# Kernel tuning notes

Measured on AMD Instinct MI355X. Metric: run time of the kernel, lower is better.

Reference implementation:

```python
import jax, jax.numpy as jnp
import numpy as np

NUM_NODES = 200000  # num_user + num_item
DIM_E = 64
NUM_EDGES = 600000
EPS = 1e-12
NEG_SLOPE = 0.01  # F.leaky_relu default


def setup_inputs() -> dict:
    key = jax.random.key(0)
    k1, k2, k3 = jax.random.split(key, 3)
    # xavier_normal on [N, D]: std = sqrt(2/(fan_in+fan_out))
    std = float(np.sqrt(2.0 / (NUM_NODES + DIM_E)))
    id_embedding = jax.random.normal(k1, (NUM_NODES, DIM_E), dtype=jnp.float32) * std
    edge_index = jax.random.randint(k2, (2, NUM_EDGES), 0, NUM_NODES, dtype=jnp.int64)
    weight_vector = jax.random.uniform(k3, (2 * NUM_EDGES, 1), dtype=jnp.float32)
    return {"id_embedding": id_embedding, "edge_index": edge_index,
            "weight_vector": weight_vector}


def _l2_normalize(x):
    # F.normalize(x, p=2, dim=1, eps=1e-12)
    n = jnp.sqrt(jnp.sum(x * x, axis=1, keepdims=True))
    return x / jnp.maximum(n, EPS)


def _leaky_relu(x):
    return jnp.where(x >= 0, x, NEG_SLOPE * x)


def reference(id_embedding, edge_index, weight_vector):
    N = id_embedding.shape[0]
    # symmetrize: cat(edge_index, edge_index[[1,0]])
    ei = jnp.concatenate([edge_index, edge_index[::-1]], axis=1)
    src, dst = ei[0], ei[1]  # messages flow src -> dst (PyG source_to_target)
    cnt = jax.ops.segment_sum(jnp.ones((src.shape[0],), jnp.float32), dst,
                              num_segments=N)[:, None]
    denom = jnp.maximum(cnt, 1.0)  # isolated nodes: sum is 0, mean defined as 0

    def conv(x):
        msg = x[src] * weight_vector            # gather + per-edge scale [2E, D]
        agg = jax.ops.segment_sum(msg, dst, num_segments=N)  # scatter-sum [N, D]
        return agg / denom                      # scatter-mean

    x = _l2_normalize(id_embedding)
    x1 = _leaky_relu(conv(x))
    x2 = _leaky_relu(conv(x1))
    return x + x1 + x2
```

## Files before the change

kernel.cpp:

```cpp
#include <hip/hip_runtime.h>
#include <hip/hip_fp16.h>

#define DIM 64
#define NEG_SLOPE 0.01f
#define BKT 256
#define TILEP 4096
#define RECS (TILEP * 2)
#define STILE 2048

typedef unsigned u32;
typedef unsigned short u16;
typedef unsigned char u8;


__global__ void k_norm_hist(const float* __restrict__ emb,
                            __half* __restrict__ x0h,
                            const int* __restrict__ p,
                            u32* __restrict__ mat,
                            int N, int E, int rb, int B, int nblkE) {
    int t = threadIdx.x;
    if ((int)blockIdx.x < rb) {
        int lane = t & 63;
        int row  = blockIdx.x * 32 + (t >> 6) * 4 + (lane >> 4);
        int l16  = lane & 15;
        if (row >= N) return;
        float4 v = *(const float4*)(emb + (size_t)row * DIM + l16 * 4);
        float s = v.x * v.x + v.y * v.y + v.z * v.z + v.w * v.w;
        #pragma unroll
        for (int m = 1; m < 16; m <<= 1) s += __shfl_xor(s, m, 64);
        float inv = 1.0f / fmaxf(sqrtf(s), 1e-12f);
        union { uint2 u; __half2 h[2]; } pk;
        pk.h[0] = __floats2half2_rn(v.x * inv, v.y * inv);
        pk.h[1] = __floats2half2_rn(v.z * inv, v.w * inv);
        *(uint2*)(x0h + (size_t)row * DIM + l16 * 4) = pk.u;
    } else {
        __shared__ u32 hist[800];
        int blk = blockIdx.x - rb;
        for (int i = t; i < B; i += 512) hist[i] = 0;
        __syncthreads();
        int base = blk * TILEP;
        #pragma unroll
        for (int k = 0; k < TILEP / 512; k++) {
            int pe = base + k * 512 + t;
            if (pe < E) {
                int a = p[pe];
                int b = p[pe + E];
                atomicAdd(&hist[(u32)b >> 8], 1u);
                atomicAdd(&hist[(u32)a >> 8], 1u);
            }
        }
        __syncthreads();
        for (int i = t; i < B; i += 512) mat[(size_t)i * nblkE + blk] = hist[i];
    }
}

__global__ void k_scan1(const u32* __restrict__ in, u32* __restrict__ out,
                        u32* __restrict__ bsum, int M) {
    __shared__ u32 sdata[256];
    int t = threadIdx.x;
    int base = blockIdx.x * STILE + t * 8;
    u32 v[8]; u32 tsum = 0;
    #pragma unroll
    for (int k = 0; k < 8; k++) {
        int i = base + k;
        v[k] = (i < M) ? in[i] : 0u;
        tsum += v[k];
    }
    sdata[t] = tsum;
    __syncthreads();
    for (int off = 1; off < 256; off <<= 1) {
        u32 x = (t >= off) ? sdata[t - off] : 0u;
        __syncthreads();
        sdata[t] += x;
        __syncthreads();
    }
    u32 run = sdata[t] - tsum;
    if (t == 255) bsum[blockIdx.x] = sdata[255];
    #pragma unroll
    for (int k = 0; k < 8; k++) {
        int i = base + k;
        if (i < M) out[i] = run;
        run += v[k];
    }
}

__global__ void k_scanfix(u32* __restrict__ mscan,
                          const u32* __restrict__ bsum, int nb, int M) {
    __shared__ u32 sdata[256];
    __shared__ u32 sexcl[256];
    int t = threadIdx.x;
    u32 v = (t < nb) ? bsum[t] : 0u;
    sdata[t] = v;
    __syncthreads();
    for (int off = 1; off < 256; off <<= 1) {
        u32 x = (t >= off) ? sdata[t - off] : 0u;
        __syncthreads();
        sdata[t] += x;
        __syncthreads();
    }
    sexcl[t] = sdata[t] - v;
    __syncthreads();
    int i = blockIdx.x * 256 + t;
    if (i < M) mscan[i] += sexcl[i >> 11];
}

__global__ __launch_bounds__(512, 1)
void k_place(const int* __restrict__ p, const float* __restrict__ w,
             const u32* __restrict__ mscan,
             u32* __restrict__ pay, u8* __restrict__ loc8,
             int E, int nblkE, int B) {
    __shared__ u32 sPay[RECS];
    __shared__ u32 sMeta[RECS];
    __shared__ u16 sPerm[RECS];
    __shared__ u32 hist[1024];
    __shared__ u32 sstart[1024];
    __shared__ u32 delta[1024];
    __shared__ u32 sdata[512];

    int blk = blockIdx.x;
    int t = threadIdx.x;
    int base = blk * TILEP;
    int rem = E - base;
    int vlim = rem * 2; if (vlim > RECS) vlim = RECS;

    hist[t] = 0; hist[t + 512] = 0;
    __syncthreads();

    #pragma unroll
    for (int k = 0; k < TILEP / 512; k++) {
        int pe = base + k * 512 + t;
        if (pe < E) {
            int a = p[pe];
            int b = p[pe + E];
            float wf = w[pe];
            float wb = w[pe + E];
            u32 wf14 = (u32)(wf * 16384.0f + 0.5f); if (wf14 > 16383u) wf14 = 16383u;
            u32 wb14 = (u32)(wb * 16384.0f + 0.5f); if (wb14 > 16383u) wb14 = 16383u;
            int li = (k * 512 + t) * 2;
            sPay[li]      = ((u32)a << 14) | wf14;
            sMeta[li]     = (u32)b;
            sPay[li + 1]  = ((u32)b << 14) | wb14;
            sMeta[li + 1] = (u32)a;
            atomicAdd(&hist[(u32)b >> 8], 1u);
            atomicAdd(&hist[(u32)a >> 8], 1u);
        }
    }
    __syncthreads();

    u32 a0 = hist[2 * t], a1 = hist[2 * t + 1];
    u32 tsum = a0 + a1;
    sdata[t] = tsum;
    __syncthreads();
    for (int off = 1; off < 512; off <<= 1) {
        u32 x = (t >= off) ? sdata[t - off] : 0u;
        __syncthreads();
        sdata[t] += x;
        __syncthreads();
    }
    u32 texcl = sdata[t] - tsum;
    sstart[2 * t]     = texcl;
    sstart[2 * t + 1] = texcl + a0;
    __syncthreads();

    hist[t] = 0; hist[t + 512] = 0;
    for (int i = t; i < B; i += 512)
        delta[i] = mscan[(size_t)i * nblkE + blk] - sstart[i];
    __syncthreads();

    #pragma unroll
    for (int k = 0; k < RECS / 512; k++) {
        int li = k * 512 + t;
        if (li < vlim) {
            u32 bin = sMeta[li] >> 8;
            u32 r = atomicAdd(&hist[bin], 1u);
            sPerm[sstart[bin] + r] = (u16)li;
        }
    }
    __syncthreads();

    #pragma unroll
    for (int k = 0; k < RECS / 512; k++) {
        int j = k * 512 + t;
        if (j < vlim) {
            int li = sPerm[j];
            u32 pv = sPay[li];
            u32 mt = sMeta[li];
            u32 gs = (u32)j + delta[mt >> 8];
            pay[gs]  = pv;
            loc8[gs] = (u8)(mt & 255u);
        }
    }
}

__global__ void k_bucket(const u32* __restrict__ pay,
                         const u8* __restrict__ loc8,
                         const u32* __restrict__ mscan,
                         u32* __restrict__ row_ptr,
                         u32* __restrict__ colw,
                         int N, int E, int B, int nblkE) {
    __shared__ u32 hist[BKT];
    __shared__ u32 excl[BKT];
    __shared__ u32 sdata[256];
    int b = blockIdx.x;
    int t = threadIdx.x;
    int node0 = b * BKT;
    int nnodes = N - node0; if (nnodes > BKT) nnodes = BKT;
    size_t flat0 = (size_t)b * nblkE;
    u32 seg_s = mscan[flat0];
    u32 seg_e = (b + 1 < B) ? mscan[flat0 + nblkE] : (u32)(2 * E);
    hist[t] = 0;
    __syncthreads();
    for (u32 j = seg_s + t; j < seg_e; j += 256)
        atomicAdd(&hist[loc8[j]], 1u);
    __syncthreads();
    u32 tsum = hist[t];
    sdata[t] = tsum;
    __syncthreads();
    for (int off = 1; off < 256; off <<= 1) {
        u32 x = (t >= off) ? sdata[t - off] : 0u;
        __syncthreads();
        sdata[t] += x;
        __syncthreads();
    }
    u32 texcl = sdata[t] - tsum;
    excl[t] = texcl;
    if (t < nnodes) row_ptr[node0 + t] = seg_s + texcl;
    if (b == 0 && t == 0) row_ptr[N] = (u32)(2 * E);
    __syncthreads();
    for (u32 j = seg_s + t; j < seg_e; j += 256) {
        u32 loc = loc8[j];
        u32 pos = atomicAdd(&excl[loc], 1u);
        colw[seg_s + pos] = pay[j];
    }
}


__device__ __forceinline__ void gather8(const __half* __restrict__ x,
                                        const u32* __restrict__ colw,
                                        u32 s, u32 e, int g, int sub,
                                        float acc[8]) {
    for (u32 base = s; base < e; base += 8) {
        int m = (int)(e - base); if (m > 8) m = 8;
        u32 u = 0;
        if (sub < m) u = colw[base + sub];
        int   cx = (int)(u >> 14);
        float cy = (float)(u & 16383u) * (1.0f / 16384.0f);
        for (int j = 0; j < m; j++) {
            int   sj = __shfl(cx, (g << 3) | j, 64);
            float wj = __shfl(cy, (g << 3) | j, 64);
            uint4 q = *(const uint4*)(x + (size_t)sj * DIM + sub * 8);
            const __half2* hp = (const __half2*)&q;
            #pragma unroll
            for (int k = 0; k < 4; k++) {
                float2 f = __half22float2(hp[k]);
                acc[2 * k]     += f.x * wj;
                acc[2 * k + 1] += f.y * wj;
            }
        }
    }
}

__global__ void k_conv1(const __half* __restrict__ x0h,
                        const u32* __restrict__ row_ptr,
                        const u32* __restrict__ colw,
                        __half* __restrict__ x1h, int N) {
    int wave = (blockIdx.x * 256 + threadIdx.x) >> 6;
    int g    = (threadIdx.x >> 3) & 7;
    int sub  = threadIdx.x & 7;
    int row  = wave * 8 + g;
    if (row >= N) return;
    u32 s = row_ptr[row], e = row_ptr[row + 1];
    float acc[8] = {0, 0, 0, 0, 0, 0, 0, 0};
    gather8(x0h, colw, s, e, g, sub, acc);
    float rdeno = 1.0f / fmaxf((float)(e - s), 1.0f);
    __half2 hv[4];
    #pragma unroll
    for (int k = 0; k < 4; k++) {
        float v0 = acc[2 * k] * rdeno;
        float v1 = acc[2 * k + 1] * rdeno;
        v0 = (v0 >= 0.0f) ? v0 : NEG_SLOPE * v0;
        v1 = (v1 >= 0.0f) ? v1 : NEG_SLOPE * v1;
        hv[k] = __floats2half2_rn(v0, v1);
    }
    *(uint4*)(x1h + (size_t)row * DIM + sub * 8) = *(const uint4*)hv;
}

__global__ void k_conv2(const __half* __restrict__ x0h,
                        const __half* __restrict__ x1h,
                        const u32* __restrict__ row_ptr,
                        const u32* __restrict__ colw,
                        float* __restrict__ out, int N) {
    int wave = (blockIdx.x * 256 + threadIdx.x) >> 6;
    int g    = (threadIdx.x >> 3) & 7;
    int sub  = threadIdx.x & 7;
    int row  = wave * 8 + g;
    if (row >= N) return;
    u32 s = row_ptr[row], e = row_ptr[row + 1];
    float acc[8] = {0, 0, 0, 0, 0, 0, 0, 0};
    gather8(x1h, colw, s, e, g, sub, acc);
    float rdeno = 1.0f / fmaxf((float)(e - s), 1.0f);
    uint4 q0 = *(const uint4*)(x0h + (size_t)row * DIM + sub * 8);
    uint4 q1 = *(const uint4*)(x1h + (size_t)row * DIM + sub * 8);
    const __half2* h0 = (const __half2*)&q0;
    const __half2* h1 = (const __half2*)&q1;
    float r[8];
    #pragma unroll
    for (int k = 0; k < 4; k++) {
        float2 a = __half22float2(h0[k]);
        float2 b = __half22float2(h1[k]);
        float x2a = acc[2 * k] * rdeno;
        float x2b = acc[2 * k + 1] * rdeno;
        x2a = (x2a >= 0.0f) ? x2a : NEG_SLOPE * x2a;
        x2b = (x2b >= 0.0f) ? x2b : NEG_SLOPE * x2b;
        r[2 * k]     = a.x + b.x + x2a;
        r[2 * k + 1] = a.y + b.y + x2b;
    }
    float* op = out + (size_t)row * DIM + sub * 8;
    *(float4*)(op)     = make_float4(r[0], r[1], r[2], r[3]);
    *(float4*)(op + 4) = make_float4(r[4], r[5], r[6], r[7]);
}

static inline size_t align16(size_t x) { return (x + 15) & ~(size_t)15; }

extern "C" void kernel_launch(void* const* d_in, const int* in_sizes, int n_in,
                              void* d_out, int out_size, void* d_ws, size_t ws_size,
                              hipStream_t stream) {
    const int N = in_sizes[0] / DIM;
    const int E = in_sizes[1] / 2;

    const float* emb = (const float*)d_in[0];
    const int*   ei  = (const int*)d_in[1];
    const float* w   = (const float*)d_in[2];
    float*       out = (float*)d_out;

    const int B     = (N + BKT - 1) / BKT;
    const int nblkE = (E + TILEP - 1) / TILEP;
    const int M     = B * nblkE;
    const int nb1   = (M + STILE - 1) / STILE;
    const int rb    = (N + 31) / 32;
    const int cvb   = (N + 31) / 32;

    char* ws = (char*)d_ws;
    size_t off = 0;
    __half* x0h    = (__half*)(ws + off); off += align16((size_t)N * DIM * 2);
    __half* x1h    = (__half*)(ws + off); off += align16((size_t)N * DIM * 2);
    u32*    pay    = (u32*)(ws + off);    off += align16((size_t)2 * E * 4);
    u8*     loc8   = (u8*)(ws + off);     off += align16((size_t)2 * E);
    u32*    colw   = (u32*)(ws + off);    off += align16((size_t)2 * E * 4);
    u32*    mat    = (u32*)(ws + off);    off += align16((size_t)M * 4);
    u32*    mscan  = (u32*)(ws + off);    off += align16((size_t)M * 4);
    u32*    row_ptr= (u32*)(ws + off);    off += align16((size_t)(N + 1) * 4);
    u32*    bsum   = (u32*)(ws + off);    off += align16(256 * 4);

    k_norm_hist<<<rb + nblkE, 512, 0, stream>>>(emb, x0h, ei, mat, N, E, rb, B, nblkE);
    k_scan1  <<<nb1, 256, 0, stream>>>(mat, mscan, bsum, M);
    k_scanfix<<<(M + 255) / 256, 256, 0, stream>>>(mscan, bsum, nb1, M);
    k_place  <<<nblkE, 512, 0, stream>>>(ei, w, mscan, pay, loc8, E, nblkE, B);
    k_bucket <<<B, 256, 0, stream>>>(pay, loc8, mscan, row_ptr, colw, N, E, B, nblkE);

    k_conv1<<<cvb, 256, 0, stream>>>(x0h, row_ptr, colw, x1h, N);
    k_conv2<<<cvb, 256, 0, stream>>>(x0h, x1h, row_ptr, colw, out, N);
}
```

Before: 210.7 us.

## Sort rows by degree for balanced conv waves and unroll gather loads

Adds a degree histogram in the bucket kernel, a scan, and a counting-sort kernel that produces a row order grouped by degree, so each wave's eight rows have similar neighbour counts in both conv kernels. The gather loop now issues all eight neighbour loads before the FMAs, and conv2 hoists its self-row loads ahead of the gather, to raise memory-level parallelism. This adds two small kernels, an order indirection, and scattered output writes. It also always loads eight neighbours even when fewer are valid, reading padded index 0 with weight 0.

```diff
diff --git a/kernel.cpp b/kernel.cpp
--- a/kernel.cpp
+++ b/kernel.cpp
@@ -85,10 +85,12 @@
 }
 
 __global__ void k_scanfix(u32* __restrict__ mscan,
-                          const u32* __restrict__ bsum, int nb, int M) {
+                          const u32* __restrict__ bsum,
+                          u32* __restrict__ dhist, int nb, int M) {
     __shared__ u32 sdata[256];
     __shared__ u32 sexcl[256];
     int t = threadIdx.x;
+    if (blockIdx.x == 0) dhist[t] = 0;
     u32 v = (t < nb) ? bsum[t] : 0u;
     sdata[t] = v;
     __syncthreads();
@@ -197,10 +199,12 @@
                          const u32* __restrict__ mscan,
                          u32* __restrict__ row_ptr,
                          u32* __restrict__ colw,
+                         u32* __restrict__ dhist,
                          int N, int E, int B, int nblkE) {
     __shared__ u32 hist[BKT];
     __shared__ u32 excl[BKT];
     __shared__ u32 sdata[256];
+    __shared__ u32 dh[256];
     int b = blockIdx.x;
     int t = threadIdx.x;
     int node0 = b * BKT;
@@ -209,11 +213,13 @@
     u32 seg_s = mscan[flat0];
     u32 seg_e = (b + 1 < B) ? mscan[flat0 + nblkE] : (u32)(2 * E);
     hist[t] = 0;
+    dh[t] = 0;
     __syncthreads();
     for (u32 j = seg_s + t; j < seg_e; j += 256)
         atomicAdd(&hist[loc8[j]], 1u);
     __syncthreads();
     u32 tsum = hist[t];
+    if (t < nnodes) atomicAdd(&dh[tsum > 255u ? 255u : tsum], 1u);
     sdata[t] = tsum;
     __syncthreads();
     for (int off = 1; off < 256; off <<= 1) {
@@ -227,6 +233,7 @@
     if (t < nnodes) row_ptr[node0 + t] = seg_s + texcl;
     if (b == 0 && t == 0) row_ptr[N] = (u32)(2 * E);
     __syncthreads();
+    if (dh[t]) atomicAdd(&dhist[t], dh[t]);
     for (u32 j = seg_s + t; j < seg_e; j += 256) {
         u32 loc = loc8[j];
         u32 pos = atomicAdd(&excl[loc], 1u);
@@ -234,41 +241,113 @@
     }
 }
 
+__global__ void k_dscan(const u32* __restrict__ dhist, u32* __restrict__ dcur) {
+    __shared__ u32 sdata[256];
+    int t = threadIdx.x;
+    u32 v = dhist[t];
+    sdata[t] = v;
+    __syncthreads();
+    for (int off = 1; off < 256; off <<= 1) {
+        u32 x = (t >= off) ? sdata[t - off] : 0u;
+        __syncthreads();
+        sdata[t] += x;
+        __syncthreads();
+    }
+    dcur[t] = sdata[t] - v;
+}
+
+__global__ void k_dorder(const u32* __restrict__ rp, u32* __restrict__ dcur,
+                         u32* __restrict__ order, int N) {
+    __shared__ u32 lh[256];
+    __shared__ u32 lbase[256];
+    __shared__ u32 lcur[256];
+    int t = threadIdx.x;
+    lh[t] = 0;
+    __syncthreads();
+    int base = blockIdx.x * 2048;
+    u32 degv[8];
+    #pragma unroll
+    for (int k = 0; k < 8; k++) {
+        int i = base + k * 256 + t;
+        u32 d = 0;
+        if (i < N) {
+            d = rp[i + 1] - rp[i];
+            if (d > 255u) d = 255u;
+            atomicAdd(&lh[d], 1u);
+        }
+        degv[k] = d;
+    }
+    __syncthreads();
+    u32 c = lh[t];
+    lbase[t] = c ? atomicAdd(&dcur[t], c) : 0u;
+    lcur[t] = 0;
+    __syncthreads();
+    #pragma unroll
+    for (int k = 0; k < 8; k++) {
+        int i = base + k * 256 + t;
+        if (i < N) {
+            u32 d = degv[k];
+            u32 r = atomicAdd(&lcur[d], 1u);
+            order[lbase[d] + r] = (u32)i;
+        }
+    }
+}
+
+
+__device__ __forceinline__ void fma8(const uint4& q, float wj, float acc[8]) {
+    const __half2* hp = (const __half2*)&q;
+    #pragma unroll
+    for (int k = 0; k < 4; k++) {
+        float2 f = __half22float2(hp[k]);
+        acc[2 * k]     += f.x * wj;
+        acc[2 * k + 1] += f.y * wj;
+    }
+}
 
 __device__ __forceinline__ void gather8(const __half* __restrict__ x,
                                         const u32* __restrict__ colw,
                                         u32 s, u32 e, int g, int sub,
                                         float acc[8]) {
+    int lb = g << 3;
     for (u32 base = s; base < e; base += 8) {
         int m = (int)(e - base); if (m > 8) m = 8;
-        u32 u = 0;
-        if (sub < m) u = colw[base + sub];
+        u32 u = (sub < m) ? colw[base + sub] : 0u;
         int   cx = (int)(u >> 14);
         float cy = (float)(u & 16383u) * (1.0f / 16384.0f);
-        for (int j = 0; j < m; j++) {
-            int   sj = __shfl(cx, (g << 3) | j, 64);
-            float wj = __shfl(cy, (g << 3) | j, 64);
-            uint4 q = *(const uint4*)(x + (size_t)sj * DIM + sub * 8);
-            const __half2* hp = (const __half2*)&q;
-            #pragma unroll
-            for (int k = 0; k < 4; k++) {
-                float2 f = __half22float2(hp[k]);
-                acc[2 * k]     += f.x * wj;
-                acc[2 * k + 1] += f.y * wj;
-            }
-        }
+        int s0 = __shfl(cx, lb + 0, 64), s1 = __shfl(cx, lb + 1, 64);
+        int s2 = __shfl(cx, lb + 2, 64), s3 = __shfl(cx, lb + 3, 64);
+        int s4 = __shfl(cx, lb + 4, 64), s5 = __shfl(cx, lb + 5, 64);
+        int s6 = __shfl(cx, lb + 6, 64), s7 = __shfl(cx, lb + 7, 64);
+        uint4 q0 = *(const uint4*)(x + (size_t)s0 * DIM + sub * 8);
+        uint4 q1 = *(const uint4*)(x + (size_t)s1 * DIM + sub * 8);
+        uint4 q2 = *(const uint4*)(x + (size_t)s2 * DIM + sub * 8);
+        uint4 q3 = *(const uint4*)(x + (size_t)s3 * DIM + sub * 8);
+        uint4 q4 = *(const uint4*)(x + (size_t)s4 * DIM + sub * 8);
+        uint4 q5 = *(const uint4*)(x + (size_t)s5 * DIM + sub * 8);
+        uint4 q6 = *(const uint4*)(x + (size_t)s6 * DIM + sub * 8);
+        uint4 q7 = *(const uint4*)(x + (size_t)s7 * DIM + sub * 8);
+        float w0 = __shfl(cy, lb + 0, 64), w1 = __shfl(cy, lb + 1, 64);
+        float w2 = __shfl(cy, lb + 2, 64), w3 = __shfl(cy, lb + 3, 64);
+        float w4 = __shfl(cy, lb + 4, 64), w5 = __shfl(cy, lb + 5, 64);
+        float w6 = __shfl(cy, lb + 6, 64), w7 = __shfl(cy, lb + 7, 64);
+        fma8(q0, w0, acc); fma8(q1, w1, acc);
+        fma8(q2, w2, acc); fma8(q3, w3, acc);
+        fma8(q4, w4, acc); fma8(q5, w5, acc);
+        fma8(q6, w6, acc); fma8(q7, w7, acc);
     }
 }
 
 __global__ void k_conv1(const __half* __restrict__ x0h,
                         const u32* __restrict__ row_ptr,
                         const u32* __restrict__ colw,
+                        const u32* __restrict__ order,
                         __half* __restrict__ x1h, int N) {
     int wave = (blockIdx.x * 256 + threadIdx.x) >> 6;
     int g    = (threadIdx.x >> 3) & 7;
     int sub  = threadIdx.x & 7;
-    int row  = wave * 8 + g;
-    if (row >= N) return;
+    int idx  = wave * 8 + g;
+    if (idx >= N) return;
+    int row = (int)order[idx];
     u32 s = row_ptr[row], e = row_ptr[row + 1];
     float acc[8] = {0, 0, 0, 0, 0, 0, 0, 0};
     gather8(x0h, colw, s, e, g, sub, acc);
@@ -289,18 +368,20 @@
                         const __half* __restrict__ x1h,
                         const u32* __restrict__ row_ptr,
                         const u32* __restrict__ colw,
+                        const u32* __restrict__ order,
                         float* __restrict__ out, int N) {
     int wave = (blockIdx.x * 256 + threadIdx.x) >> 6;
     int g    = (threadIdx.x >> 3) & 7;
     int sub  = threadIdx.x & 7;
-    int row  = wave * 8 + g;
-    if (row >= N) return;
+    int idx  = wave * 8 + g;
+    if (idx >= N) return;
+    int row = (int)order[idx];
     u32 s = row_ptr[row], e = row_ptr[row + 1];
+    uint4 q0 = *(const uint4*)(x0h + (size_t)row * DIM + sub * 8);
+    uint4 q1 = *(const uint4*)(x1h + (size_t)row * DIM + sub * 8);
     float acc[8] = {0, 0, 0, 0, 0, 0, 0, 0};
     gather8(x1h, colw, s, e, g, sub, acc);
     float rdeno = 1.0f / fmaxf((float)(e - s), 1.0f);
-    uint4 q0 = *(const uint4*)(x0h + (size_t)row * DIM + sub * 8);
-    uint4 q1 = *(const uint4*)(x1h + (size_t)row * DIM + sub * 8);
     const __half2* h0 = (const __half2*)&q0;
     const __half2* h1 = (const __half2*)&q1;
     float r[8];
@@ -339,6 +420,7 @@
     const int nb1   = (M + STILE - 1) / STILE;
     const int rb    = (N + 31) / 32;
     const int cvb   = (N + 31) / 32;
+    const int ob    = (N + 2047) / 2048;
 
     char* ws = (char*)d_ws;
     size_t off = 0;
@@ -351,13 +433,18 @@
     u32*    mscan  = (u32*)(ws + off);    off += align16((size_t)M * 4);
     u32*    row_ptr= (u32*)(ws + off);    off += align16((size_t)(N + 1) * 4);
     u32*    bsum   = (u32*)(ws + off);    off += align16(256 * 4);
+    u32*    dhist  = (u32*)(ws + off);    off += align16(256 * 4);
+    u32*    dcur   = (u32*)(ws + off);    off += align16(256 * 4);
+    u32*    order  = (u32*)(ws + off);    off += align16((size_t)N * 4);
 
     k_norm_hist<<<rb + nblkE, 512, 0, stream>>>(emb, x0h, ei, mat, N, E, rb, B, nblkE);
     k_scan1  <<<nb1, 256, 0, stream>>>(mat, mscan, bsum, M);
-    k_scanfix<<<(M + 255) / 256, 256, 0, stream>>>(mscan, bsum, nb1, M);
+    k_scanfix<<<(M + 255) / 256, 256, 0, stream>>>(mscan, bsum, dhist, nb1, M);
     k_place  <<<nblkE, 512, 0, stream>>>(ei, w, mscan, pay, loc8, E, nblkE, B);
-    k_bucket <<<B, 256, 0, stream>>>(pay, loc8, mscan, row_ptr, colw, N, E, B, nblkE);
-
-    k_conv1<<<cvb, 256, 0, stream>>>(x0h, row_ptr, colw, x1h, N);
-    k_conv2<<<cvb, 256, 0, stream>>>(x0h, x1h, row_ptr, colw, out, N);
-}
+    k_bucket <<<B, 256, 0, stream>>>(pay, loc8, mscan, row_ptr, colw, dhist, N, E, B, nblkE);
+    k_dscan  <<<1, 256, 0, stream>>>(dhist, dcur);
+    k_dorder <<<ob, 256, 0, stream>>>(row_ptr, dcur, order, N);
+
+    k_conv1<<<cvb, 256, 0, stream>>>(x0h, row_ptr, colw, order, x1h, N);
+    k_conv2<<<cvb, 256, 0, stream>>>(x0h, x1h, row_ptr, colw, order, out, N);
+}
```

New measurement: 226.8 us. 1.08x slower.

## Process two rows per lane group with batched unrolled neighbor gathers

Applied to the files above, without the earlier changes.

Each 8-lane group in both conv kernels now owns two destination rows instead of one. The neighbor loop is fully unrolled to issue eight independent 16-byte row loads (four per row) before any FMA, replacing the serial per-neighbor load-then-accumulate loop. This exposes more memory-level parallelism in the latency-bound gather and halves the launched grid. The cost is padded lanes: when a row has fewer than eight remaining edges, the extra lanes still load node 0 with zero weight, and register use per thread rises.

```diff
diff --git a/kernel.cpp b/kernel.cpp
--- a/kernel.cpp
+++ b/kernel.cpp
@@ -235,28 +235,66 @@
 }
 
 
-__device__ __forceinline__ void gather8(const __half* __restrict__ x,
+__device__ __forceinline__ void fma8(const uint4& q, float wj, float acc[8]) {
+    const __half2* hp = (const __half2*)&q;
+    #pragma unroll
+    for (int k = 0; k < 4; k++) {
+        float2 f = __half22float2(hp[k]);
+        acc[2 * k]     += f.x * wj;
+        acc[2 * k + 1] += f.y * wj;
+    }
+}
+
+__device__ __forceinline__ void gather2(const __half* __restrict__ x,
                                         const u32* __restrict__ colw,
-                                        u32 s, u32 e, int g, int sub,
-                                        float acc[8]) {
-    for (u32 base = s; base < e; base += 8) {
-        int m = (int)(e - base); if (m > 8) m = 8;
-        u32 u = 0;
-        if (sub < m) u = colw[base + sub];
-        int   cx = (int)(u >> 14);
-        float cy = (float)(u & 16383u) * (1.0f / 16384.0f);
-        for (int j = 0; j < m; j++) {
-            int   sj = __shfl(cx, (g << 3) | j, 64);
-            float wj = __shfl(cy, (g << 3) | j, 64);
-            uint4 q = *(const uint4*)(x + (size_t)sj * DIM + sub * 8);
-            const __half2* hp = (const __half2*)&q;
-            #pragma unroll
-            for (int k = 0; k < 4; k++) {
-                float2 f = __half22float2(hp[k]);
-                acc[2 * k]     += f.x * wj;
-                acc[2 * k + 1] += f.y * wj;
-            }
+                                        u32 s0, u32 e0, u32 s1, u32 e1,
+                                        int g, int sub,
+                                        float accA[8], float accB[8]) {
+    int lb = g << 3;
+    u32 bA = s0, bB = s1;
+    while (bA < e0 || bB < e1) {
+        u32 uA = (bA + (u32)sub < e0 && bA < e0) ? colw[bA + sub] : 0u;
+        u32 uB = (bB + (u32)sub < e1 && bB < e1) ? colw[bB + sub] : 0u;
+        int   cxA = (int)(uA >> 14);
+        float cyA = (float)(uA & 16383u) * (1.0f / 16384.0f);
+        int   cxB = (int)(uB >> 14);
+        float cyB = (float)(uB & 16383u) * (1.0f / 16384.0f);
+        #pragma unroll
+        for (int h = 0; h < 2; h++) {
+            int j0 = h * 4;
+            int a0 = __shfl(cxA, lb + j0 + 0, 64), a1 = __shfl(cxA, lb + j0 + 1, 64);
+            int a2 = __shfl(cxA, lb + j0 + 2, 64), a3 = __shfl(cxA, lb + j0 + 3, 64);
+            int b0 = __shfl(cxB, lb + j0 + 0, 64), b1 = __shfl(cxB, lb + j0 + 1, 64);
+            int b2 = __shfl(cxB, lb + j0 + 2, 64), b3 = __shfl(cxB, lb + j0 + 3, 64);
+            uint4 qa0 = *(const uint4*)(x + (size_t)a0 * DIM + sub * 8);
+            uint4 qa1 = *(const uint4*)(x + (size_t)a1 * DIM + sub * 8);
+            uint4 qa2 = *(const uint4*)(x + (size_t)a2 * DIM + sub * 8);
+            uint4 qa3 = *(const uint4*)(x + (size_t)a3 * DIM + sub * 8);
+            uint4 qb0 = *(const uint4*)(x + (size_t)b0 * DIM + sub * 8);
+            uint4 qb1 = *(const uint4*)(x + (size_t)b1 * DIM + sub * 8);
+            uint4 qb2 = *(const uint4*)(x + (size_t)b2 * DIM + sub * 8);
+            uint4 qb3 = *(const uint4*)(x + (size_t)b3 * DIM + sub * 8);
+            float wa0 = __shfl(cyA, lb + j0 + 0, 64), wa1 = __shfl(cyA, lb + j0 + 1, 64);
+            float wa2 = __shfl(cyA, lb + j0 + 2, 64), wa3 = __shfl(cyA, lb + j0 + 3, 64);
+            float wb0 = __shfl(cyB, lb + j0 + 0, 64), wb1 = __shfl(cyB, lb + j0 + 1, 64);
+            float wb2 = __shfl(cyB, lb + j0 + 2, 64), wb3 = __shfl(cyB, lb + j0 + 3, 64);
+            fma8(qa0, wa0, accA); fma8(qa1, wa1, accA);
+            fma8(qa2, wa2, accA); fma8(qa3, wa3, accA);
+            fma8(qb0, wb0, accB); fma8(qb1, wb1, accB);
+            fma8(qb2, wb2, accB); fma8(qb3, wb3, accB);
         }
+        bA += 8; bB += 8;
+    }
+}
+
+__device__ __forceinline__ void finish1(float acc[8], float rdeno, __half2 hv[4]) {
+    #pragma unroll
+    for (int k = 0; k < 4; k++) {
+        float v0 = acc[2 * k] * rdeno;
+        float v1 = acc[2 * k + 1] * rdeno;
+        v0 = (v0 >= 0.0f) ? v0 : NEG_SLOPE * v0;
+        v1 = (v1 >= 0.0f) ? v1 : NEG_SLOPE * v1;
+        hv[k] = __floats2half2_rn(v0, v1);
     }
 }
 
@@ -267,43 +305,28 @@
     int wave = (blockIdx.x * 256 + threadIdx.x) >> 6;
     int g    = (threadIdx.x >> 3) & 7;
     int sub  = threadIdx.x & 7;
-    int row  = wave * 8 + g;
-    if (row >= N) return;
-    u32 s = row_ptr[row], e = row_ptr[row + 1];
-    float acc[8] = {0, 0, 0, 0, 0, 0, 0, 0};
-    gather8(x0h, colw, s, e, g, sub, acc);
-    float rdeno = 1.0f / fmaxf((float)(e - s), 1.0f);
+    int r0   = wave * 16 + g * 2;
+    int r1   = r0 + 1;
+    if (r0 >= N) return;
+    u32 s0 = row_ptr[r0], e0 = row_ptr[r0 + 1];
+    u32 s1 = 0, e1 = 0;
+    if (r1 < N) { s1 = row_ptr[r1]; e1 = row_ptr[r1 + 1]; }
+    float accA[8] = {0,0,0,0,0,0,0,0};
+    float accB[8] = {0,0,0,0,0,0,0,0};
+    gather2(x0h, colw, s0, e0, s1, e1, g, sub, accA, accB);
     __half2 hv[4];
-    #pragma unroll
-    for (int k = 0; k < 4; k++) {
-        float v0 = acc[2 * k] * rdeno;
-        float v1 = acc[2 * k + 1] * rdeno;
-        v0 = (v0 >= 0.0f) ? v0 : NEG_SLOPE * v0;
-        v1 = (v1 >= 0.0f) ? v1 : NEG_SLOPE * v1;
-        hv[k] = __floats2half2_rn(v0, v1);
-    }
-    *(uint4*)(x1h + (size_t)row * DIM + sub * 8) = *(const uint4*)hv;
-}
-
-__global__ void k_conv2(const __half* __restrict__ x0h,
-                        const __half* __restrict__ x1h,
-                        const u32* __restrict__ row_ptr,
-                        const u32* __restrict__ colw,
-                        float* __restrict__ out, int N) {
-    int wave = (blockIdx.x * 256 + threadIdx.x) >> 6;
-    int g    = (threadIdx.x >> 3) & 7;
-    int sub  = threadIdx.x & 7;
-    int row  = wave * 8 + g;
-    if (row >= N) return;
-    u32 s = row_ptr[row], e = row_ptr[row + 1];
-    float acc[8] = {0, 0, 0, 0, 0, 0, 0, 0};
-    gather8(x1h, colw, s, e, g, sub, acc);
-    float rdeno = 1.0f / fmaxf((float)(e - s), 1.0f);
-    uint4 q0 = *(const uint4*)(x0h + (size_t)row * DIM + sub * 8);
-    uint4 q1 = *(const uint4*)(x1h + (size_t)row * DIM + sub * 8);
+    finish1(accA, 1.0f / fmaxf((float)(e0 - s0), 1.0f), hv);
+    *(uint4*)(x1h + (size_t)r0 * DIM + sub * 8) = *(const uint4*)hv;
+    if (r1 < N) {
+        finish1(accB, 1.0f / fmaxf((float)(e1 - s1), 1.0f), hv);
+        *(uint4*)(x1h + (size_t)r1 * DIM + sub * 8) = *(const uint4*)hv;
+    }
+}
+
+__device__ __forceinline__ void finish2(const uint4& q0, const uint4& q1,
+                                        float acc[8], float rdeno, float r[8]) {
     const __half2* h0 = (const __half2*)&q0;
     const __half2* h1 = (const __half2*)&q1;
-    float r[8];
     #pragma unroll
     for (int k = 0; k < 4; k++) {
         float2 a = __half22float2(h0[k]);
@@ -315,9 +338,43 @@
         r[2 * k]     = a.x + b.x + x2a;
         r[2 * k + 1] = a.y + b.y + x2b;
     }
-    float* op = out + (size_t)row * DIM + sub * 8;
+}
+
+__global__ void k_conv2(const __half* __restrict__ x0h,
+                        const __half* __restrict__ x1h,
+                        const u32* __restrict__ row_ptr,
+                        const u32* __restrict__ colw,
+                        float* __restrict__ out, int N) {
+    int wave = (blockIdx.x * 256 + threadIdx.x) >> 6;
+    int g    = (threadIdx.x >> 3) & 7;
+    int sub  = threadIdx.x & 7;
+    int r0   = wave * 16 + g * 2;
+    int r1   = r0 + 1;
+    if (r0 >= N) return;
+    u32 s0 = row_ptr[r0], e0 = row_ptr[r0 + 1];
+    u32 s1 = 0, e1 = 0;
+    if (r1 < N) { s1 = row_ptr[r1]; e1 = row_ptr[r1 + 1]; }
+    uint4 qa0 = *(const uint4*)(x0h + (size_t)r0 * DIM + sub * 8);
+    uint4 qa1 = *(const uint4*)(x1h + (size_t)r0 * DIM + sub * 8);
+    uint4 qb0, qb1;
+    if (r1 < N) {
+        qb0 = *(const uint4*)(x0h + (size_t)r1 * DIM + sub * 8);
+        qb1 = *(const uint4*)(x1h + (size_t)r1 * DIM + sub * 8);
+    }
+    float accA[8] = {0,0,0,0,0,0,0,0};
+    float accB[8] = {0,0,0,0,0,0,0,0};
+    gather2(x1h, colw, s0, e0, s1, e1, g, sub, accA, accB);
+    float r[8];
+    finish2(qa0, qa1, accA, 1.0f / fmaxf((float)(e0 - s0), 1.0f), r);
+    float* op = out + (size_t)r0 * DIM + sub * 8;
     *(float4*)(op)     = make_float4(r[0], r[1], r[2], r[3]);
     *(float4*)(op + 4) = make_float4(r[4], r[5], r[6], r[7]);
+    if (r1 < N) {
+        finish2(qb0, qb1, accB, 1.0f / fmaxf((float)(e1 - s1), 1.0f), r);
+        op = out + (size_t)r1 * DIM + sub * 8;
+        *(float4*)(op)     = make_float4(r[0], r[1], r[2], r[3]);
+        *(float4*)(op + 4) = make_float4(r[4], r[5], r[6], r[7]);
+    }
 }
 
 static inline size_t align16(size_t x) { return (x + 15) & ~(size_t)15; }
@@ -338,7 +395,7 @@
     const int M     = B * nblkE;
     const int nb1   = (M + STILE - 1) / STILE;
     const int rb    = (N + 31) / 32;
-    const int cvb   = (N + 31) / 32;
+    const int cvb   = (N + 63) / 64;
 
     char* ws = (char*)d_ws;
     size_t off = 0;
```

Measured after the change: 220.5 us. 1.05x slower.

## Fold scan fixup into place/bucket kernels, halve place tile, stage bucket in LDS

Applied to the files above, without the earlier changes.

Removes the separate scan-fixup kernel by having k_place and k_bucket each rescan the block sums and add the offset on the fly. This saves one launch and one read-modify-write pass over the scan matrix. It also halves the k_place tile so four blocks can fit per CU instead of one, and stages up to 2048 payload and loc records per bucket in LDS to avoid reading global memory twice. In conv2 the self-row loads move before the gather to overlap latency. Halving TILEP doubles nblkE and M, so the scan work and the per-block bsum rescans grow, and sbsE only covers 128 block sums.

```diff
diff --git a/kernel.cpp b/kernel.cpp
--- a/kernel.cpp
+++ b/kernel.cpp
@@ -4,7 +4,7 @@
 #define DIM 64
 #define NEG_SLOPE 0.01f
 #define BKT 256
-#define TILEP 4096
+#define TILEP 2048
 #define RECS (TILEP * 2)
 #define STILE 2048
 
@@ -84,38 +84,19 @@
     }
 }
 
-__global__ void k_scanfix(u32* __restrict__ mscan,
-                          const u32* __restrict__ bsum, int nb, int M) {
-    __shared__ u32 sdata[256];
-    __shared__ u32 sexcl[256];
-    int t = threadIdx.x;
-    u32 v = (t < nb) ? bsum[t] : 0u;
-    sdata[t] = v;
-    __syncthreads();
-    for (int off = 1; off < 256; off <<= 1) {
-        u32 x = (t >= off) ? sdata[t - off] : 0u;
-        __syncthreads();
-        sdata[t] += x;
-        __syncthreads();
-    }
-    sexcl[t] = sdata[t] - v;
-    __syncthreads();
-    int i = blockIdx.x * 256 + t;
-    if (i < M) mscan[i] += sexcl[i >> 11];
-}
-
-__global__ __launch_bounds__(512, 1)
+__global__ __launch_bounds__(512, 4)
 void k_place(const int* __restrict__ p, const float* __restrict__ w,
-             const u32* __restrict__ mscan,
+             const u32* __restrict__ mscan, const u32* __restrict__ bsum,
              u32* __restrict__ pay, u8* __restrict__ loc8,
-             int E, int nblkE, int B) {
+             int E, int nblkE, int B, int nb1) {
     __shared__ u32 sPay[RECS];
     __shared__ u32 sMeta[RECS];
     __shared__ u16 sPerm[RECS];
     __shared__ u32 hist[1024];
     __shared__ u32 sstart[1024];
-    __shared__ u32 delta[1024];
+    __shared__ u32 delta[800];
     __shared__ u32 sdata[512];
+    __shared__ u32 sbsE[128];
 
     int blk = blockIdx.x;
     int t = threadIdx.x;
@@ -123,6 +104,16 @@
     int rem = E - base;
     int vlim = rem * 2; if (vlim > RECS) vlim = RECS;
 
+    u32 bv = (t < nb1) ? bsum[t] : 0u;
+    sdata[t] = bv;
+    __syncthreads();
+    for (int off = 1; off < 512; off <<= 1) {
+        u32 x = (t >= off) ? sdata[t - off] : 0u;
+        __syncthreads();
+        sdata[t] += x;
+        __syncthreads();
+    }
+    if (t < 128) sbsE[t] = sdata[t] - bv;
     hist[t] = 0; hist[t + 512] = 0;
     __syncthreads();
 
@@ -163,8 +154,10 @@
     __syncthreads();
 
     hist[t] = 0; hist[t + 512] = 0;
-    for (int i = t; i < B; i += 512)
-        delta[i] = mscan[(size_t)i * nblkE + blk] - sstart[i];
+    for (int i = t; i < B; i += 512) {
+        size_t fi = (size_t)i * nblkE + blk;
+        delta[i] = mscan[fi] + sbsE[fi >> 11] - sstart[i];
+    }
     __syncthreads();
 
     #pragma unroll
@@ -195,23 +188,51 @@
 __global__ void k_bucket(const u32* __restrict__ pay,
                          const u8* __restrict__ loc8,
                          const u32* __restrict__ mscan,
+                         const u32* __restrict__ bsum,
                          u32* __restrict__ row_ptr,
                          u32* __restrict__ colw,
-                         int N, int E, int B, int nblkE) {
+                         int N, int E, int B, int nblkE, int nb1) {
     __shared__ u32 hist[BKT];
     __shared__ u32 excl[BKT];
     __shared__ u32 sdata[256];
+    __shared__ u32 sexc[256];
+    __shared__ u32 spay[2048];
+    __shared__ u8  sloc[2048];
     int b = blockIdx.x;
     int t = threadIdx.x;
     int node0 = b * BKT;
     int nnodes = N - node0; if (nnodes > BKT) nnodes = BKT;
+
+    u32 bv = (t < nb1) ? bsum[t] : 0u;
+    sdata[t] = bv;
+    __syncthreads();
+    for (int off = 1; off < 256; off <<= 1) {
+        u32 x = (t >= off) ? sdata[t - off] : 0u;
+        __syncthreads();
+        sdata[t] += x;
+        __syncthreads();
+    }
+    sexc[t] = sdata[t] - bv;
+    __syncthreads();
+
     size_t flat0 = (size_t)b * nblkE;
-    u32 seg_s = mscan[flat0];
-    u32 seg_e = (b + 1 < B) ? mscan[flat0 + nblkE] : (u32)(2 * E);
+    u32 seg_s = mscan[flat0] + sexc[flat0 >> 11];
+    u32 seg_e = (b + 1 < B) ? (mscan[flat0 + nblkE] + sexc[(flat0 + nblkE) >> 11])
+                            : (u32)(2 * E);
+    u32 span = seg_e - seg_s;
+    u32 nst  = span < 2048u ? span : 2048u;
+
     hist[t] = 0;
     __syncthreads();
-    for (u32 j = seg_s + t; j < seg_e; j += 256)
-        atomicAdd(&hist[loc8[j]], 1u);
+    for (u32 j = t; j < nst; j += 256) {
+        spay[j] = pay[seg_s + j];
+        sloc[j] = loc8[seg_s + j];
+    }
+    __syncthreads();
+    for (u32 j = t; j < span; j += 256) {
+        u32 loc = (j < nst) ? (u32)sloc[j] : (u32)loc8[seg_s + j];
+        atomicAdd(&hist[loc], 1u);
+    }
     __syncthreads();
     u32 tsum = hist[t];
     sdata[t] = tsum;
@@ -227,10 +248,12 @@
     if (t < nnodes) row_ptr[node0 + t] = seg_s + texcl;
     if (b == 0 && t == 0) row_ptr[N] = (u32)(2 * E);
     __syncthreads();
-    for (u32 j = seg_s + t; j < seg_e; j += 256) {
-        u32 loc = loc8[j];
+    for (u32 j = t; j < span; j += 256) {
+        u32 loc, pv;
+        if (j < nst) { loc = sloc[j]; pv = spay[j]; }
+        else         { loc = loc8[seg_s + j]; pv = pay[seg_s + j]; }
         u32 pos = atomicAdd(&excl[loc], 1u);
-        colw[seg_s + pos] = pay[j];
+        colw[seg_s + pos] = pv;
     }
 }
 
@@ -296,11 +319,11 @@
     int row  = wave * 8 + g;
     if (row >= N) return;
     u32 s = row_ptr[row], e = row_ptr[row + 1];
+    uint4 q0 = *(const uint4*)(x0h + (size_t)row * DIM + sub * 8);
+    uint4 q1 = *(const uint4*)(x1h + (size_t)row * DIM + sub * 8);
     float acc[8] = {0, 0, 0, 0, 0, 0, 0, 0};
     gather8(x1h, colw, s, e, g, sub, acc);
     float rdeno = 1.0f / fmaxf((float)(e - s), 1.0f);
-    uint4 q0 = *(const uint4*)(x0h + (size_t)row * DIM + sub * 8);
-    uint4 q1 = *(const uint4*)(x1h + (size_t)row * DIM + sub * 8);
     const __half2* h0 = (const __half2*)&q0;
     const __half2* h1 = (const __half2*)&q1;
     float r[8];
@@ -353,10 +376,9 @@
     u32*    bsum   = (u32*)(ws + off);    off += align16(256 * 4);
 
     k_norm_hist<<<rb + nblkE, 512, 0, stream>>>(emb, x0h, ei, mat, N, E, rb, B, nblkE);
-    k_scan1  <<<nb1, 256, 0, stream>>>(mat, mscan, bsum, M);
-    k_scanfix<<<(M + 255) / 256, 256, 0, stream>>>(mscan, bsum, nb1, M);
-    k_place  <<<nblkE, 512, 0, stream>>>(ei, w, mscan, pay, loc8, E, nblkE, B);
-    k_bucket <<<B, 256, 0, stream>>>(pay, loc8, mscan, row_ptr, colw, N, E, B, nblkE);
+    k_scan1 <<<nb1, 256, 0, stream>>>(mat, mscan, bsum, M);
+    k_place <<<nblkE, 512, 0, stream>>>(ei, w, mscan, bsum, pay, loc8, E, nblkE, B, nb1);
+    k_bucket<<<B, 256, 0, stream>>>(pay, loc8, mscan, bsum, row_ptr, colw, N, E, B, nblkE, nb1);
 
     k_conv1<<<cvb, 256, 0, stream>>>(x0h, row_ptr, colw, x1h, N);
     k_conv2<<<cvb, 256, 0, stream>>>(x0h, x1h, row_ptr, colw, out, N);
```

Result: no change. 209.1 us (-0.7%).
